# Kernel tuning notes

Measured on AMD Instinct MI355X. Metric: run time of the kernel, lower is better.

Reference implementation:

```python
import jax, jax.numpy as jnp
import numpy as np

N, E = 50000, 800000
F_IN, H = 64, 64
DEPTH, LAYERS = 3, 2


def setup_inputs() -> dict:
    key = jax.random.key(0)
    ks = jax.random.split(key, 14)
    z = jax.random.normal(ks[0], (N, F_IN), dtype=jnp.float32)
    edge_index = jax.random.randint(ks[1], (2, E), 0, N, dtype=jnp.int64)
    s = 1.0 / np.sqrt(H)
    u = lambda k, shape: jax.random.uniform(k, shape, jnp.float32, -s, s)
    return dict(
        z=z, edge_index=edge_index,
        # GRU layer 0 (input F_IN), torch gate order r,z,n
        W_ih0=u(ks[2], (3 * H, F_IN)), W_hh0=u(ks[3], (3 * H, H)),
        b_ih0=u(ks[4], (3 * H,)), b_hh0=u(ks[5], (3 * H,)),
        # GRU layer 1 (input H)
        W_ih1=u(ks[6], (3 * H, H)), W_hh1=u(ks[7], (3 * H, H)),
        b_ih1=u(ks[8], (3 * H,)), b_hh1=u(ks[9], (3 * H,)),
        # output head: Tanh -> Linear(H, 1)
        W_out=u(ks[10], (1, H)), b_out=u(ks[11], (1,)),
    )


def _mean_aggr(h, src, dst, n_nodes):
    # scatter-mean of neighbor (src) states into dst nodes
    msg = jax.ops.segment_sum(h[src], dst, num_segments=n_nodes)  # [N, F]
    cnt = jax.ops.segment_sum(jnp.ones((src.shape[0],), h.dtype), dst,
                              num_segments=n_nodes)
    return msg / jnp.maximum(cnt, 1.0)[:, None]


def _gru_cell(x, h, W_ih, W_hh, b_ih, b_hh):
    gi = x @ W_ih.T + b_ih          # [N, 3H]
    gh = h @ W_hh.T + b_hh
    i_r, i_z, i_n = jnp.split(gi, 3, axis=-1)
    h_r, h_z, h_n = jnp.split(gh, 3, axis=-1)
    r = jax.nn.sigmoid(i_r + h_r)
    zt = jax.nn.sigmoid(i_z + h_z)
    n = jnp.tanh(i_n + r * h_n)
    return (1.0 - zt) * n + zt * h


def _run_gru_layer(xs, W_ih, W_hh, b_ih, b_hh):
    # xs: [T, N, F]; returns (outputs [T, N, H], last hidden [N, H])
    h0 = jnp.zeros((xs.shape[1], W_hh.shape[1]), xs.dtype)

    def step(h, x):
        h2 = _gru_cell(x, h, W_ih, W_hh, b_ih, b_hh)
        return h2, h2

    hT, ys = jax.lax.scan(step, h0, xs)
    return ys, hT


def reference(z, edge_index, W_ih0, W_hh0, b_ih0, b_hh0,
              W_ih1, W_hh1, b_ih1, b_hh1, W_out, b_out):
    src, dst = edge_index[0], edge_index[1]
    n_nodes = z.shape[0]
    # Build the tree-depth sequence: original z followed by DEPTH rounds of
    # mean message passing (irregular gather-aggregate-scatter per depth).
    seq = [z]
    h = z
    for _ in range(DEPTH):
        h = _mean_aggr(h, src, dst, n_nodes)
        seq.append(h)
    xs = jnp.stack(seq, axis=0)  # [DEPTH+1, N, F_IN]
    ys, _ = _run_gru_layer(xs, W_ih0, W_hh0, b_ih0, b_hh0)
    _, hT = _run_gru_layer(ys, W_ih1, W_hh1, b_ih1, b_hh1)  # top layer final state
    return jnp.tanh(hT) @ W_out.T + b_out  # [N, 1]
```

## Files before the change

kernel.cpp:

```cpp
#include <hip/hip_runtime.h>
#include <hip/hip_bf16.h>

#define N_NODES 50000
#define N_EDGES 800000

typedef __attribute__((ext_vector_type(8))) short short8;
typedef __attribute__((ext_vector_type(4))) float f32x4;

__device__ __forceinline__ unsigned short f2bf_hi(float f) {
    unsigned u = __float_as_uint(f);
    unsigned r = u + 0x7fffu + ((u >> 16) & 1u);
    return (unsigned short)(r >> 16);
}
__device__ __forceinline__ float bf2f(unsigned short h) {
    return __uint_as_float(((unsigned)h) << 16);
}
__device__ __forceinline__ float u2f(unsigned u) { return __uint_as_float(u); }

__device__ __forceinline__ unsigned pack_bf2(float a, float b) {
    float2 t{a, b};
    __hip_bfloat162 r = __float22bfloat162_rn(t);
    return *reinterpret_cast<unsigned*>(&r);
}

__device__ __forceinline__ float sigm_(float v) {
    return __builtin_amdgcn_rcpf(1.0f + __expf(-v));
}
__device__ __forceinline__ float tanh2_(float a) {
    float e = __expf(-2.0f * a);
    return fmaf(2.0f, __builtin_amdgcn_rcpf(1.0f + e), -1.0f);
}


__global__ __launch_bounds__(256) void count_kernel(const int* __restrict__ ei,
                                                    int* __restrict__ deg) {
    int e = blockIdx.x * 256 + threadIdx.x;
    if (e < N_EDGES) atomicAdd(&deg[ei[N_EDGES + e]], 1);
}

__global__ __launch_bounds__(256) void scan_part(const int* __restrict__ deg,
                                                 int* __restrict__ part) {
    __shared__ int sm[256];
    int b = blockIdx.x, t = threadIdx.x;
    int s = 0;
#pragma unroll
    for (int i = 0; i < 4; ++i) {
        int idx = b * 1024 + i * 256 + t;
        if (idx < N_NODES) s += deg[idx];
    }
    sm[t] = s;
    __syncthreads();
    for (int off = 128; off; off >>= 1) {
        if (t < off) sm[t] += sm[t + off];
        __syncthreads();
    }
    if (t == 0) part[b] = sm[0];
}

__global__ __launch_bounds__(1024) void scan_final(const int* __restrict__ deg,
                                                   const int* __restrict__ part,
                                                   int* __restrict__ rowptr,
                                                   int* __restrict__ cur) {
    __shared__ int sm[1024];
    __shared__ int basep;
    int b = blockIdx.x, t = threadIdx.x;
    if (t < 64) {
        int v = (t < b) ? part[t] : 0;
#pragma unroll
        for (int off = 1; off < 64; off <<= 1) v += __shfl_xor(v, off);
        if (t == 0) basep = v;
    }
    int idx = b * 1024 + t;
    int d = (idx < N_NODES) ? deg[idx] : 0;
    sm[t] = d;
    __syncthreads();
    for (int off = 1; off < 1024; off <<= 1) {
        int u = (t >= off) ? sm[t - off] : 0;
        __syncthreads();
        sm[t] += u;
        __syncthreads();
    }
    int excl = basep + sm[t] - d;
    if (idx < N_NODES) {
        rowptr[idx] = excl;
        cur[idx] = excl;
    } else if (idx == N_NODES) {
        rowptr[idx] = excl;
    }
}

__global__ __launch_bounds__(256) void fill_kernel(const int* __restrict__ ei,
                                                   int* __restrict__ cur,
                                                   int* __restrict__ col) {
    int e = blockIdx.x * 256 + threadIdx.x;
    if (e < N_EDGES) {
        int s = ei[e];
        int d = ei[N_EDGES + e];
        int p = atomicAdd(&cur[d], 1);
        col[p] = s;
    }
}


__global__ __launch_bounds__(256) void gather_f32_kernel(
    const int* __restrict__ rowptr, const int* __restrict__ col,
    const float* __restrict__ src,
    unsigned short* __restrict__ dsthi, unsigned short* __restrict__ dstlo) {
    int node = (blockIdx.x * 256 + threadIdx.x) >> 6;
    if (node >= N_NODES) return;
    const int lane = threadIdx.x & 63;
    const int g = lane >> 4;
    const int l16 = lane & 15;
    const int beg = rowptr[node], end = rowptr[node + 1];
    const float4* s4 = reinterpret_cast<const float4*>(src);

    float4 a0 = {0.f, 0.f, 0.f, 0.f}, a1 = {0.f, 0.f, 0.f, 0.f};
    float4 a2 = {0.f, 0.f, 0.f, 0.f}, a3 = {0.f, 0.f, 0.f, 0.f};
#pragma unroll 1
    for (int e = beg + 4 * g; e < end; e += 16) {
        float4 v0 = s4[col[e] * 16 + l16];
        a0.x += v0.x; a0.y += v0.y; a0.z += v0.z; a0.w += v0.w;
        if (e + 1 < end) {
            float4 v1 = s4[col[e + 1] * 16 + l16];
            a1.x += v1.x; a1.y += v1.y; a1.z += v1.z; a1.w += v1.w;
        }
        if (e + 2 < end) {
            float4 v2 = s4[col[e + 2] * 16 + l16];
            a2.x += v2.x; a2.y += v2.y; a2.z += v2.z; a2.w += v2.w;
        }
        if (e + 3 < end) {
            float4 v3 = s4[col[e + 3] * 16 + l16];
            a3.x += v3.x; a3.y += v3.y; a3.z += v3.z; a3.w += v3.w;
        }
    }
    a0.x += a1.x; a0.y += a1.y; a0.z += a1.z; a0.w += a1.w;
    a2.x += a3.x; a2.y += a3.y; a2.z += a3.z; a2.w += a3.w;
    a0.x += a2.x; a0.y += a2.y; a0.z += a2.z; a0.w += a2.w;
#pragma unroll
    for (int m = 16; m <= 32; m <<= 1) {
        a0.x += __shfl_xor(a0.x, m);
        a0.y += __shfl_xor(a0.y, m);
        a0.z += __shfl_xor(a0.z, m);
        a0.w += __shfl_xor(a0.w, m);
    }
    if (g == 0) {
        float inv = __builtin_amdgcn_rcpf(fmaxf((float)(end - beg), 1.0f));
        float m0 = a0.x * inv, m1 = a0.y * inv, m2 = a0.z * inv, m3 = a0.w * inv;
        unsigned h01 = pack_bf2(m0, m1), h23 = pack_bf2(m2, m3);
        float l0 = m0 - u2f(h01 << 16), l1 = m1 - u2f(h01 & 0xffff0000u);
        float l2 = m2 - u2f(h23 << 16), l3 = m3 - u2f(h23 & 0xffff0000u);
        uint2 hw = {h01, h23};
        uint2 lw = {pack_bf2(l0, l1), pack_bf2(l2, l3)};
        reinterpret_cast<uint2*>(dsthi)[node * 16 + l16] = hw;
        reinterpret_cast<uint2*>(dstlo)[node * 16 + l16] = lw;
    }
}


__global__ __launch_bounds__(256) void gather_bf16_kernel(
    const int* __restrict__ rowptr, const int* __restrict__ col,
    const unsigned short* __restrict__ srchi,
    unsigned short* __restrict__ dsthi, unsigned short* __restrict__ dstlo) {
    int node = (blockIdx.x * 256 + threadIdx.x) >> 6;
    if (node >= N_NODES) return;
    const int lane = threadIdx.x & 63;
    const int g = lane >> 4;
    const int l16 = lane & 15;
    const int beg = rowptr[node], end = rowptr[node + 1];
    const uint2* s2 = reinterpret_cast<const uint2*>(srchi);

    float b0 = 0.f, b1 = 0.f, b2 = 0.f, b3 = 0.f;
    float c0 = 0.f, c1 = 0.f, c2 = 0.f, c3 = 0.f;
#pragma unroll 1
    for (int e = beg + 2 * g; e < end; e += 8) {
        uint2 v = s2[col[e] * 16 + l16];
        b0 += u2f(v.x << 16); b1 += u2f(v.x & 0xffff0000u);
        b2 += u2f(v.y << 16); b3 += u2f(v.y & 0xffff0000u);
        if (e + 1 < end) {
            uint2 w = s2[col[e + 1] * 16 + l16];
            c0 += u2f(w.x << 16); c1 += u2f(w.x & 0xffff0000u);
            c2 += u2f(w.y << 16); c3 += u2f(w.y & 0xffff0000u);
        }
    }
    b0 += c0; b1 += c1; b2 += c2; b3 += c3;
#pragma unroll
    for (int m = 16; m <= 32; m <<= 1) {
        b0 += __shfl_xor(b0, m);
        b1 += __shfl_xor(b1, m);
        b2 += __shfl_xor(b2, m);
        b3 += __shfl_xor(b3, m);
    }
    if (g == 0) {
        float inv = __builtin_amdgcn_rcpf(fmaxf((float)(end - beg), 1.0f));
        float m0 = b0 * inv, m1 = b1 * inv, m2 = b2 * inv, m3 = b3 * inv;
        unsigned h01 = pack_bf2(m0, m1), h23 = pack_bf2(m2, m3);
        float l0 = m0 - u2f(h01 << 16), l1 = m1 - u2f(h01 & 0xffff0000u);
        float l2 = m2 - u2f(h23 << 16), l3 = m3 - u2f(h23 & 0xffff0000u);
        uint2 hw = {h01, h23};
        uint2 lw = {pack_bf2(l0, l1), pack_bf2(l2, l3)};
        reinterpret_cast<uint2*>(dsthi)[node * 16 + l16] = hw;
        reinterpret_cast<uint2*>(dstlo)[node * 16 + l16] = lw;
    }
}


__global__ __launch_bounds__(256) void wprep_kernel(
    const float* __restrict__ Wih0, const float* __restrict__ Whh0,
    const float* __restrict__ Wih1, const float* __restrict__ Whh1,
    unsigned short* __restrict__ wout) {
    int idx = blockIdx.x * 256 + threadIdx.x;
    if (idx >= 49152) return;
    int e = idx & 7;
    int lane = (idx >> 3) & 63;
    int ks = (idx >> 9) & 1;
    int r = idx >> 10;
    int ct = r % 12;
    int mat = (r / 12) & 1;
    int layer = r / 24;
    const float* W = layer ? (mat ? Whh1 : Wih1) : (mat ? Whh0 : Wih0);
    int j = ct * 16 + (lane & 15);
    int k = ks * 32 + ((lane >> 4) << 3) + e;
    float v = W[j * 64 + k];
    unsigned short hi = f2bf_hi(v);
    unsigned short lo = f2bf_hi(v - bf2f(hi));
    int base = layer * 49152 + mat * 24576 + ct * 2048 + ks * 1024;
    wout[base + lane * 8 + e] = hi;
    wout[base + 512 + lane * 8 + e] = lo;
}


__device__ __forceinline__ f32x4 mfma_bf16(short8 a, short8 b, f32x4 c) {
    return __builtin_amdgcn_mfma_f32_16x16x32_bf16(a, b, c, 0, 0, 0);
}

__device__ __forceinline__ short8 lds_read8(const unsigned short* p) {
    union { uint2 u[2]; short8 s; } t;
    t.u[0] = *reinterpret_cast<const uint2*>(p);
    t.u[1] = *reinterpret_cast<const uint2*>(p + 4);
    return t.s;
}

#define HPAD 76

template <int LAYER>
__device__ __forceinline__ void mfma_phase(
    int ct, int col16, int kgrp,
    const short8 (&wf)[2][2][2][2],
    float bias_a, float bias_b,
    const unsigned short (*Ahi)[HPAD], const unsigned short (*Alo)[HPAD],
    unsigned short (&Hhi)[2][32][HPAD], unsigned short (&Hlo)[2][32][HPAD],
    float (&G)[32][196], float (&Gn2)[32][68]) {
    f32x4 acc_a[2], acc_b[2];
#pragma unroll
    for (int rt = 0; rt < 2; ++rt) {
        acc_a[rt] = {bias_a, bias_a, bias_a, bias_a};
        acc_b[rt] = {bias_b, bias_b, bias_b, bias_b};
    }
#pragma unroll
    for (int rt = 0; rt < 2; ++rt) {
#pragma unroll
        for (int ks = 0; ks < 2; ++ks) {
            const int row = rt * 16 + col16;
            const int koff = ks * 32 + kgrp;
            short8 a_in_hi = lds_read8(&Ahi[row][koff]);
            short8 a_in_lo = lds_read8(&Alo[row][koff]);
            short8 a_h_hi = lds_read8(&Hhi[LAYER][row][koff]);
            short8 a_h_lo = lds_read8(&Hlo[LAYER][row][koff]);
            short8 bi0 = wf[LAYER][0][ks][0], bi1 = wf[LAYER][0][ks][1];
            short8 bh0 = wf[LAYER][1][ks][0], bh1 = wf[LAYER][1][ks][1];
            acc_a[rt] = mfma_bf16(a_in_hi, bi0, acc_a[rt]);
            acc_a[rt] = mfma_bf16(a_in_hi, bi1, acc_a[rt]);
            acc_a[rt] = mfma_bf16(a_in_lo, bi0, acc_a[rt]);
            if (ct < 8) {
                acc_a[rt] = mfma_bf16(a_h_hi, bh0, acc_a[rt]);
                acc_a[rt] = mfma_bf16(a_h_hi, bh1, acc_a[rt]);
                acc_a[rt] = mfma_bf16(a_h_lo, bh0, acc_a[rt]);
            } else {
                acc_b[rt] = mfma_bf16(a_h_hi, bh0, acc_b[rt]);
                acc_b[rt] = mfma_bf16(a_h_hi, bh1, acc_b[rt]);
                acc_b[rt] = mfma_bf16(a_h_lo, bh0, acc_b[rt]);
            }
        }
    }
    const int q4 = (kgrp >> 3) * 4;
    const int gcol = ct * 16 + col16;
#pragma unroll
    for (int rt = 0; rt < 2; ++rt) {
#pragma unroll
        for (int v = 0; v < 4; ++v) {
            int grow = rt * 16 + q4 + v;
            G[grow][gcol] = acc_a[rt][v];
            if (ct >= 8) Gn2[grow][gcol - 128] = acc_b[rt][v];
        }
    }
}

template <int LAYER>
__device__ __forceinline__ void ew_pair(
    int p,
    unsigned short (&Hhi)[2][32][HPAD], unsigned short (&Hlo)[2][32][HPAD],
    float (&G)[32][196], float (&Gn2)[32][68]) {
    int m = p >> 5, j0 = (p & 31) * 2;
    float2 gr = *reinterpret_cast<const float2*>(&G[m][j0]);
    float2 gz = *reinterpret_cast<const float2*>(&G[m][64 + j0]);
    float2 gn = *reinterpret_cast<const float2*>(&G[m][128 + j0]);
    float2 gm = *reinterpret_cast<const float2*>(&Gn2[m][j0]);
    unsigned hhi = *reinterpret_cast<const unsigned*>(&Hhi[LAYER][m][j0]);
    unsigned hlo = *reinterpret_cast<const unsigned*>(&Hlo[LAYER][m][j0]);
    float hold0 = u2f(hhi << 16) + u2f(hlo << 16);
    float hold1 = u2f(hhi & 0xffff0000u) + u2f(hlo & 0xffff0000u);
    float r0 = sigm_(gr.x), r1 = sigm_(gr.y);
    float z0 = sigm_(gz.x), z1 = sigm_(gz.y);
    float n0 = tanh2_(fmaf(r0, gm.x, gn.x));
    float n1 = tanh2_(fmaf(r1, gm.y, gn.y));
    float h0 = fmaf(z0, hold0 - n0, n0);
    float h1 = fmaf(z1, hold1 - n1, n1);
    unsigned phi = pack_bf2(h0, h1);
    float l0 = h0 - u2f(phi << 16);
    float l1 = h1 - u2f(phi & 0xffff0000u);
    unsigned plo = pack_bf2(l0, l1);
    *reinterpret_cast<unsigned*>(&Hhi[LAYER][m][j0]) = phi;
    *reinterpret_cast<unsigned*>(&Hlo[LAYER][m][j0]) = plo;
}

__device__ __forceinline__ void stage_pair_f32(const float* __restrict__ xp, int nodebase,
                                               int p,
                                               unsigned short (&Xhi)[32][HPAD],
                                               unsigned short (&Xlo)[32][HPAD]) {
    int m = p >> 5, k0 = (p & 31) * 2;
    int node = nodebase + m;
    if (node >= N_NODES) node = N_NODES - 1;
    float2 v = *reinterpret_cast<const float2*>(xp + (size_t)node * 64 + k0);
    unsigned phi = pack_bf2(v.x, v.y);
    float l0 = v.x - u2f(phi << 16);
    float l1 = v.y - u2f(phi & 0xffff0000u);
    *reinterpret_cast<unsigned*>(&Xhi[m][k0]) = phi;
    *reinterpret_cast<unsigned*>(&Xlo[m][k0]) = pack_bf2(l0, l1);
}

__global__ __launch_bounds__(768) void gru_kernel(
    const float* __restrict__ z,
    const unsigned* __restrict__ xh1, const unsigned* __restrict__ xl1,
    const unsigned* __restrict__ xh2, const unsigned* __restrict__ xl2,
    const unsigned* __restrict__ xh3, const unsigned* __restrict__ xl3,
    const unsigned short* __restrict__ wprep,
    const float* __restrict__ bih0, const float* __restrict__ bhh0,
    const float* __restrict__ bih1, const float* __restrict__ bhh1,
    const float* __restrict__ Wout, const float* __restrict__ bout,
    float* __restrict__ out) {
    __shared__ __align__(16) float G[32][196];
    __shared__ __align__(16) float Gn2[32][68];
    __shared__ __align__(16) unsigned short Hhi[2][32][HPAD];
    __shared__ __align__(16) unsigned short Hlo[2][32][HPAD];
    __shared__ __align__(16) unsigned short Xhi[32][HPAD];
    __shared__ __align__(16) unsigned short Xlo[32][HPAD];

    const int tid = threadIdx.x;
    const int lane = tid & 63;
    const int ct = tid >> 6;
    const int col16 = lane & 15;
    const int kgrp = (lane >> 4) << 3;
    const int nodebase = blockIdx.x * 32;

    short8 wf[2][2][2][2];
    {
        const short8* wp = reinterpret_cast<const short8*>(wprep);
#pragma unroll
        for (int layer = 0; layer < 2; ++layer)
#pragma unroll
            for (int mat = 0; mat < 2; ++mat)
#pragma unroll
                for (int ks = 0; ks < 2; ++ks)
#pragma unroll
                    for (int term = 0; term < 2; ++term)
                        wf[layer][mat][ks][term] =
                            wp[(layer * 49152 + mat * 24576 + ct * 2048 +
                                ks * 1024 + term * 512 + lane * 8) >> 3];
    }
    const int gcol = ct * 16 + col16;
    float bias0_a, bias0_b, bias1_a, bias1_b;
    if (ct < 8) {
        bias0_a = bih0[gcol] + bhh0[gcol]; bias0_b = 0.0f;
        bias1_a = bih1[gcol] + bhh1[gcol]; bias1_b = 0.0f;
    } else {
        bias0_a = bih0[gcol]; bias0_b = bhh0[gcol];
        bias1_a = bih1[gcol]; bias1_b = bhh1[gcol];
    }

    {
        unsigned* h32 = reinterpret_cast<unsigned*>(&Hhi[0][0][0]);
        unsigned* l32 = reinterpret_cast<unsigned*>(&Hlo[0][0][0]);
        for (int i = tid; i < 2432; i += 768) {
            h32[i] = 0;
            l32[i] = 0;
        }
    }
    stage_pair_f32(z, nodebase, tid, Xhi, Xlo);
    if (tid < 256) stage_pair_f32(z, nodebase, tid + 768, Xhi, Xlo);
    __syncthreads();

#pragma unroll 1
    for (int t = 0; t < 4; ++t) {
        mfma_phase<0>(ct, col16, kgrp, wf, bias0_a, bias0_b,
                      Xhi, Xlo, Hhi, Hlo, G, Gn2);
        __syncthreads();
        ew_pair<0>(tid, Hhi, Hlo, G, Gn2);
        if (tid < 256) ew_pair<0>(tid + 768, Hhi, Hlo, G, Gn2);
        __syncthreads();
        mfma_phase<1>(ct, col16, kgrp, wf, bias1_a, bias1_b,
                      Hhi[0], Hlo[0], Hhi, Hlo, G, Gn2);
        __syncthreads();
        if (tid < 512) {
            ew_pair<1>(tid, Hhi, Hlo, G, Gn2);
            ew_pair<1>(tid + 512, Hhi, Hlo, G, Gn2);
        } else if (t < 3) {
            const unsigned* hp = (t == 0) ? xh1 : (t == 1) ? xh2 : xh3;
            const unsigned* lp = (t == 0) ? xl1 : (t == 1) ? xl2 : xl3;
            int q = tid - 512;
#pragma unroll
            for (int i = 0; i < 4; ++i) {
                int d = q + 256 * i;
                int m = d >> 5, c = d & 31;
                int node = nodebase + m;
                if (node >= N_NODES) node = N_NODES - 1;
                *reinterpret_cast<unsigned*>(&Xhi[m][2 * c]) = hp[node * 32 + c];
                *reinterpret_cast<unsigned*>(&Xlo[m][2 * c]) = lp[node * 32 + c];
            }
        }
        __syncthreads();
    }

    if (tid < 512) {
        int m = tid >> 4, l16 = tid & 15;
        float acc = 0.0f;
#pragma unroll
        for (int q = 0; q < 4; ++q) {
            int j = l16 * 4 + q;
            float h = bf2f(Hhi[1][m][j]) + bf2f(Hlo[1][m][j]);
            acc = fmaf(tanh2_(h), Wout[j], acc);
        }
        acc += __shfl_down(acc, 8, 16);
        acc += __shfl_down(acc, 4, 16);
        acc += __shfl_down(acc, 2, 16);
        acc += __shfl_down(acc, 1, 16);
        int node = nodebase + m;
        if (l16 == 0 && node < N_NODES) out[node] = acc + bout[0];
    }
}

extern "C" void kernel_launch(void* const* d_in, const int* in_sizes, int n_in,
                              void* d_out, int out_size, void* d_ws, size_t ws_size,
                              hipStream_t stream) {
    const float* z    = (const float*)d_in[0];
    const int*   ei   = (const int*)d_in[1];
    const float* Wih0 = (const float*)d_in[2];
    const float* Whh0 = (const float*)d_in[3];
    const float* bih0 = (const float*)d_in[4];
    const float* bhh0 = (const float*)d_in[5];
    const float* Wih1 = (const float*)d_in[6];
    const float* Whh1 = (const float*)d_in[7];
    const float* bih1 = (const float*)d_in[8];
    const float* bhh1 = (const float*)d_in[9];
    const float* Wout = (const float*)d_in[10];
    const float* bout = (const float*)d_in[11];
    float* out = (float*)d_out;
    unsigned* ws = (unsigned*)d_ws;

    unsigned* xh1 = ws;
    unsigned* xl1 = xh1 + 1600000;
    unsigned* xh2 = xl1 + 1600000;
    unsigned* xl2 = xh2 + 1600000;
    unsigned* xh3 = xl2 + 1600000;
    unsigned* xl3 = xh3 + 1600000;
    unsigned short* wprep = (unsigned short*)(xl3 + 1600000);
    int* rowptr = (int*)(wprep + 98304);
    int* deg    = rowptr + 50004;
    int* cur    = deg + 50000;
    int* col    = cur + 50000;
    int* part   = col + 800000;

    hipMemsetAsync(deg, 0, 50000 * sizeof(int), stream);

    wprep_kernel<<<192, 256, 0, stream>>>(Wih0, Whh0, Wih1, Whh1, wprep);
    count_kernel<<<(N_EDGES + 255) / 256, 256, 0, stream>>>(ei, deg);
    scan_part<<<49, 256, 0, stream>>>(deg, part);
    scan_final<<<49, 1024, 0, stream>>>(deg, part, rowptr, cur);
    fill_kernel<<<(N_EDGES + 255) / 256, 256, 0, stream>>>(ei, cur, col);

    gather_f32_kernel<<<(N_NODES * 64 + 255) / 256, 256, 0, stream>>>(
        rowptr, col, z, (unsigned short*)xh1, (unsigned short*)xl1);
    gather_bf16_kernel<<<(N_NODES * 64 + 255) / 256, 256, 0, stream>>>(
        rowptr, col, (const unsigned short*)xh1,
        (unsigned short*)xh2, (unsigned short*)xl2);
    gather_bf16_kernel<<<(N_NODES * 64 + 255) / 256, 256, 0, stream>>>(
        rowptr, col, (const unsigned short*)xh2,
        (unsigned short*)xh3, (unsigned short*)xl3);

    gru_kernel<<<(N_NODES + 31) / 32, 768, 0, stream>>>(
        z, xh1, xl1, xh2, xl2, xh3, xl3, wprep,
        bih0, bhh0, bih1, bhh1, Wout, bout, out);
}
```

Baseline: 374.0 us.

## Partition neighbor gather by source range to keep source rows cache-resident

The gather kernels switch to a persistent grid in which each wave owns up to seven destination nodes and sweeps the edge lists P times. Each pass only loads source rows whose index falls in one slice of the node range, so the working set of feature rows per pass is smaller and more likely to stay in L2/MALL. The cost is re-reading col indices P times, more branch divergence, and more register pressure from seven accumulators. The bf16 gather also changes its per-lane edge stride from 2 to 4.

```diff
diff --git a/kernel.cpp b/kernel.cpp
--- a/kernel.cpp
+++ b/kernel.cpp
@@ -3,6 +3,7 @@
 
 #define N_NODES 50000
 #define N_EDGES 800000
+#define GWAVES 8192
 
 typedef __attribute__((ext_vector_type(8))) short short8;
 typedef __attribute__((ext_vector_type(4))) float f32x4;
@@ -102,104 +103,175 @@
 }
 
 
-__global__ __launch_bounds__(256) void gather_f32_kernel(
+__global__ __launch_bounds__(256, 8) void gather_f32_mp(
     const int* __restrict__ rowptr, const int* __restrict__ col,
     const float* __restrict__ src,
     unsigned short* __restrict__ dsthi, unsigned short* __restrict__ dstlo) {
-    int node = (blockIdx.x * 256 + threadIdx.x) >> 6;
-    if (node >= N_NODES) return;
+    const int gwave = (blockIdx.x * 256 + threadIdx.x) >> 6;
     const int lane = threadIdx.x & 63;
     const int g = lane >> 4;
     const int l16 = lane & 15;
-    const int beg = rowptr[node], end = rowptr[node + 1];
     const float4* s4 = reinterpret_cast<const float4*>(src);
 
-    float4 a0 = {0.f, 0.f, 0.f, 0.f}, a1 = {0.f, 0.f, 0.f, 0.f};
-    float4 a2 = {0.f, 0.f, 0.f, 0.f}, a3 = {0.f, 0.f, 0.f, 0.f};
+    float4 acc[7];
+#pragma unroll
+    for (int k = 0; k < 7; ++k) acc[k] = {0.f, 0.f, 0.f, 0.f};
+
+    const int P = 4;
 #pragma unroll 1
-    for (int e = beg + 4 * g; e < end; e += 16) {
-        float4 v0 = s4[col[e] * 16 + l16];
-        a0.x += v0.x; a0.y += v0.y; a0.z += v0.z; a0.w += v0.w;
-        if (e + 1 < end) {
-            float4 v1 = s4[col[e + 1] * 16 + l16];
-            a1.x += v1.x; a1.y += v1.y; a1.z += v1.z; a1.w += v1.w;
-        }
-        if (e + 2 < end) {
-            float4 v2 = s4[col[e + 2] * 16 + l16];
-            a2.x += v2.x; a2.y += v2.y; a2.z += v2.z; a2.w += v2.w;
-        }
-        if (e + 3 < end) {
-            float4 v3 = s4[col[e + 3] * 16 + l16];
-            a3.x += v3.x; a3.y += v3.y; a3.z += v3.z; a3.w += v3.w;
-        }
-    }
-    a0.x += a1.x; a0.y += a1.y; a0.z += a1.z; a0.w += a1.w;
-    a2.x += a3.x; a2.y += a3.y; a2.z += a3.z; a2.w += a3.w;
-    a0.x += a2.x; a0.y += a2.y; a0.z += a2.z; a0.w += a2.w;
-#pragma unroll
-    for (int m = 16; m <= 32; m <<= 1) {
-        a0.x += __shfl_xor(a0.x, m);
-        a0.y += __shfl_xor(a0.y, m);
-        a0.z += __shfl_xor(a0.z, m);
-        a0.w += __shfl_xor(a0.w, m);
-    }
-    if (g == 0) {
-        float inv = __builtin_amdgcn_rcpf(fmaxf((float)(end - beg), 1.0f));
-        float m0 = a0.x * inv, m1 = a0.y * inv, m2 = a0.z * inv, m3 = a0.w * inv;
-        unsigned h01 = pack_bf2(m0, m1), h23 = pack_bf2(m2, m3);
-        float l0 = m0 - u2f(h01 << 16), l1 = m1 - u2f(h01 & 0xffff0000u);
-        float l2 = m2 - u2f(h23 << 16), l3 = m3 - u2f(h23 & 0xffff0000u);
-        uint2 hw = {h01, h23};
-        uint2 lw = {pack_bf2(l0, l1), pack_bf2(l2, l3)};
-        reinterpret_cast<uint2*>(dsthi)[node * 16 + l16] = hw;
-        reinterpret_cast<uint2*>(dstlo)[node * 16 + l16] = lw;
-    }
-}
-
-
-__global__ __launch_bounds__(256) void gather_bf16_kernel(
+    for (int p = 0; p < P; ++p) {
+        const int lo = (int)(((long long)N_NODES * p) / P);
+        const int hi = (int)(((long long)N_NODES * (p + 1)) / P);
+#pragma unroll
+        for (int k = 0; k < 7; ++k) {
+            int node = gwave + k * GWAVES;
+            if (node >= N_NODES) break;
+            const int beg = rowptr[node], end = rowptr[node + 1];
+#pragma unroll 1
+            for (int e = beg + 4 * g; e < end; e += 16) {
+                int c0 = col[e];
+                if (c0 >= lo && c0 < hi) {
+                    float4 v = s4[c0 * 16 + l16];
+                    acc[k].x += v.x; acc[k].y += v.y;
+                    acc[k].z += v.z; acc[k].w += v.w;
+                }
+                if (e + 1 < end) {
+                    int c1 = col[e + 1];
+                    if (c1 >= lo && c1 < hi) {
+                        float4 v = s4[c1 * 16 + l16];
+                        acc[k].x += v.x; acc[k].y += v.y;
+                        acc[k].z += v.z; acc[k].w += v.w;
+                    }
+                }
+                if (e + 2 < end) {
+                    int c2 = col[e + 2];
+                    if (c2 >= lo && c2 < hi) {
+                        float4 v = s4[c2 * 16 + l16];
+                        acc[k].x += v.x; acc[k].y += v.y;
+                        acc[k].z += v.z; acc[k].w += v.w;
+                    }
+                }
+                if (e + 3 < end) {
+                    int c3 = col[e + 3];
+                    if (c3 >= lo && c3 < hi) {
+                        float4 v = s4[c3 * 16 + l16];
+                        acc[k].x += v.x; acc[k].y += v.y;
+                        acc[k].z += v.z; acc[k].w += v.w;
+                    }
+                }
+            }
+        }
+    }
+#pragma unroll
+    for (int k = 0; k < 7; ++k) {
+        int node = gwave + k * GWAVES;
+        if (node >= N_NODES) break;
+        float4 a = acc[k];
+#pragma unroll
+        for (int m = 16; m <= 32; m <<= 1) {
+            a.x += __shfl_xor(a.x, m);
+            a.y += __shfl_xor(a.y, m);
+            a.z += __shfl_xor(a.z, m);
+            a.w += __shfl_xor(a.w, m);
+        }
+        if (g == 0) {
+            const int beg = rowptr[node], end = rowptr[node + 1];
+            float inv = __builtin_amdgcn_rcpf(fmaxf((float)(end - beg), 1.0f));
+            float m0 = a.x * inv, m1 = a.y * inv, m2 = a.z * inv, m3 = a.w * inv;
+            unsigned h01 = pack_bf2(m0, m1), h23 = pack_bf2(m2, m3);
+            float l0 = m0 - u2f(h01 << 16), l1 = m1 - u2f(h01 & 0xffff0000u);
+            float l2 = m2 - u2f(h23 << 16), l3 = m3 - u2f(h23 & 0xffff0000u);
+            uint2 hw = {h01, h23};
+            uint2 lw = {pack_bf2(l0, l1), pack_bf2(l2, l3)};
+            reinterpret_cast<uint2*>(dsthi)[node * 16 + l16] = hw;
+            reinterpret_cast<uint2*>(dstlo)[node * 16 + l16] = lw;
+        }
+    }
+}
+
+__global__ __launch_bounds__(256, 8) void gather_bf16_mp(
     const int* __restrict__ rowptr, const int* __restrict__ col,
     const unsigned short* __restrict__ srchi,
     unsigned short* __restrict__ dsthi, unsigned short* __restrict__ dstlo) {
-    int node = (blockIdx.x * 256 + threadIdx.x) >> 6;
-    if (node >= N_NODES) return;
+    const int gwave = (blockIdx.x * 256 + threadIdx.x) >> 6;
     const int lane = threadIdx.x & 63;
     const int g = lane >> 4;
     const int l16 = lane & 15;
-    const int beg = rowptr[node], end = rowptr[node + 1];
     const uint2* s2 = reinterpret_cast<const uint2*>(srchi);
 
-    float b0 = 0.f, b1 = 0.f, b2 = 0.f, b3 = 0.f;
-    float c0 = 0.f, c1 = 0.f, c2 = 0.f, c3 = 0.f;
+    float4 acc[7];
+#pragma unroll
+    for (int k = 0; k < 7; ++k) acc[k] = {0.f, 0.f, 0.f, 0.f};
+
+    const int P = 3;
 #pragma unroll 1
-    for (int e = beg + 2 * g; e < end; e += 8) {
-        uint2 v = s2[col[e] * 16 + l16];
-        b0 += u2f(v.x << 16); b1 += u2f(v.x & 0xffff0000u);
-        b2 += u2f(v.y << 16); b3 += u2f(v.y & 0xffff0000u);
-        if (e + 1 < end) {
-            uint2 w = s2[col[e + 1] * 16 + l16];
-            c0 += u2f(w.x << 16); c1 += u2f(w.x & 0xffff0000u);
-            c2 += u2f(w.y << 16); c3 += u2f(w.y & 0xffff0000u);
-        }
-    }
-    b0 += c0; b1 += c1; b2 += c2; b3 += c3;
-#pragma unroll
-    for (int m = 16; m <= 32; m <<= 1) {
-        b0 += __shfl_xor(b0, m);
-        b1 += __shfl_xor(b1, m);
-        b2 += __shfl_xor(b2, m);
-        b3 += __shfl_xor(b3, m);
-    }
-    if (g == 0) {
-        float inv = __builtin_amdgcn_rcpf(fmaxf((float)(end - beg), 1.0f));
-        float m0 = b0 * inv, m1 = b1 * inv, m2 = b2 * inv, m3 = b3 * inv;
-        unsigned h01 = pack_bf2(m0, m1), h23 = pack_bf2(m2, m3);
-        float l0 = m0 - u2f(h01 << 16), l1 = m1 - u2f(h01 & 0xffff0000u);
-        float l2 = m2 - u2f(h23 << 16), l3 = m3 - u2f(h23 & 0xffff0000u);
-        uint2 hw = {h01, h23};
-        uint2 lw = {pack_bf2(l0, l1), pack_bf2(l2, l3)};
-        reinterpret_cast<uint2*>(dsthi)[node * 16 + l16] = hw;
-        reinterpret_cast<uint2*>(dstlo)[node * 16 + l16] = lw;
+    for (int p = 0; p < P; ++p) {
+        const int lo = (int)(((long long)N_NODES * p) / P);
+        const int hi = (int)(((long long)N_NODES * (p + 1)) / P);
+#pragma unroll
+        for (int k = 0; k < 7; ++k) {
+            int node = gwave + k * GWAVES;
+            if (node >= N_NODES) break;
+            const int beg = rowptr[node], end = rowptr[node + 1];
+#pragma unroll 1
+            for (int e = beg + 4 * g; e < end; e += 16) {
+                int c0 = col[e];
+                if (c0 >= lo && c0 < hi) {
+                    uint2 v = s2[c0 * 16 + l16];
+                    acc[k].x += u2f(v.x << 16); acc[k].y += u2f(v.x & 0xffff0000u);
+                    acc[k].z += u2f(v.y << 16); acc[k].w += u2f(v.y & 0xffff0000u);
+                }
+                if (e + 1 < end) {
+                    int c1 = col[e + 1];
+                    if (c1 >= lo && c1 < hi) {
+                        uint2 v = s2[c1 * 16 + l16];
+                        acc[k].x += u2f(v.x << 16); acc[k].y += u2f(v.x & 0xffff0000u);
+                        acc[k].z += u2f(v.y << 16); acc[k].w += u2f(v.y & 0xffff0000u);
+                    }
+                }
+                if (e + 2 < end) {
+                    int c2 = col[e + 2];
+                    if (c2 >= lo && c2 < hi) {
+                        uint2 v = s2[c2 * 16 + l16];
+                        acc[k].x += u2f(v.x << 16); acc[k].y += u2f(v.x & 0xffff0000u);
+                        acc[k].z += u2f(v.y << 16); acc[k].w += u2f(v.y & 0xffff0000u);
+                    }
+                }
+                if (e + 3 < end) {
+                    int c3 = col[e + 3];
+                    if (c3 >= lo && c3 < hi) {
+                        uint2 v = s2[c3 * 16 + l16];
+                        acc[k].x += u2f(v.x << 16); acc[k].y += u2f(v.x & 0xffff0000u);
+                        acc[k].z += u2f(v.y << 16); acc[k].w += u2f(v.y & 0xffff0000u);
+                    }
+                }
+            }
+        }
+    }
+#pragma unroll
+    for (int k = 0; k < 7; ++k) {
+        int node = gwave + k * GWAVES;
+        if (node >= N_NODES) break;
+        float4 a = acc[k];
+#pragma unroll
+        for (int m = 16; m <= 32; m <<= 1) {
+            a.x += __shfl_xor(a.x, m);
+            a.y += __shfl_xor(a.y, m);
+            a.z += __shfl_xor(a.z, m);
+            a.w += __shfl_xor(a.w, m);
+        }
+        if (g == 0) {
+            const int beg = rowptr[node], end = rowptr[node + 1];
+            float inv = __builtin_amdgcn_rcpf(fmaxf((float)(end - beg), 1.0f));
+            float m0 = a.x * inv, m1 = a.y * inv, m2 = a.z * inv, m3 = a.w * inv;
+            unsigned h01 = pack_bf2(m0, m1), h23 = pack_bf2(m2, m3);
+            float l0 = m0 - u2f(h01 << 16), l1 = m1 - u2f(h01 & 0xffff0000u);
+            float l2 = m2 - u2f(h23 << 16), l3 = m3 - u2f(h23 & 0xffff0000u);
+            uint2 hw = {h01, h23};
+            uint2 lw = {pack_bf2(l0, l1), pack_bf2(l2, l3)};
+            reinterpret_cast<uint2*>(dsthi)[node * 16 + l16] = hw;
+            reinterpret_cast<uint2*>(dstlo)[node * 16 + l16] = lw;
+        }
     }
 }
 
@@ -487,14 +559,12 @@
     scan_final<<<49, 1024, 0, stream>>>(deg, part, rowptr, cur);
     fill_kernel<<<(N_EDGES + 255) / 256, 256, 0, stream>>>(ei, cur, col);
 
-    gather_f32_kernel<<<(N_NODES * 64 + 255) / 256, 256, 0, stream>>>(
-        rowptr, col, z, (unsigned short*)xh1, (unsigned short*)xl1);
-    gather_bf16_kernel<<<(N_NODES * 64 + 255) / 256, 256, 0, stream>>>(
-        rowptr, col, (const unsigned short*)xh1,
-        (unsigned short*)xh2, (unsigned short*)xl2);
-    gather_bf16_kernel<<<(N_NODES * 64 + 255) / 256, 256, 0, stream>>>(
-        rowptr, col, (const unsigned short*)xh2,
-        (unsigned short*)xh3, (unsigned short*)xl3);
+    gather_f32_mp<<<2048, 256, 0, stream>>>(rowptr, col, z,
+        (unsigned short*)xh1, (unsigned short*)xl1);
+    gather_bf16_mp<<<2048, 256, 0, stream>>>(rowptr, col,
+        (const unsigned short*)xh1, (unsigned short*)xh2, (unsigned short*)xl2);
+    gather_bf16_mp<<<2048, 256, 0, stream>>>(rowptr, col,
+        (const unsigned short*)xh2, (unsigned short*)xh3, (unsigned short*)xl3);
 
     gru_kernel<<<(N_NODES + 31) / 32, 768, 0, stream>>>(
         z, xh1, xl1, xh2, xl2, xh3, xl3, wprep,
```

New measurement: 507.6 us. 35.7% more time.

## Split gather feature arrays into column slabs to shrink per-pass working set

Applied to the files above, without the earlier changes.

Node features are reorganised into column slabs (16 floats or 16 packed bf16 pairs per node per slab), and each gather pass processes one slab at a time across separate block ranges. This is meant to make the randomly accessed source slab small enough to stay resident in cache while neighbors are gathered, cutting DRAM traffic from irregular reads. It adds a transpose kernel for z, more blocks and narrower per-lane loads, repeated reads of rowptr/col per slab, and a slab-addressed load in the GRU kernel.

```diff
diff --git a/kernel.cpp b/kernel.cpp
--- a/kernel.cpp
+++ b/kernel.cpp
@@ -3,6 +3,7 @@
 
 #define N_NODES 50000
 #define N_EDGES 800000
+#define SLABU 800000
 
 typedef __attribute__((ext_vector_type(8))) short short8;
 typedef __attribute__((ext_vector_type(4))) float f32x4;
@@ -102,104 +103,97 @@
 }
 
 
-__global__ __launch_bounds__(256) void gather_f32_kernel(
+__global__ __launch_bounds__(256) void zslab_kernel(const float* __restrict__ z,
+                                                    float* __restrict__ zs) {
+    int idx = blockIdx.x * 256 + threadIdx.x;
+    if (idx < N_NODES * 64) {
+        int node = idx >> 6, f = idx & 63;
+        zs[(f >> 4) * SLABU + node * 16 + (f & 15)] = z[idx];
+    }
+}
+
+
+__global__ __launch_bounds__(256) void gather_f32_slab(
     const int* __restrict__ rowptr, const int* __restrict__ col,
-    const float* __restrict__ src,
-    unsigned short* __restrict__ dsthi, unsigned short* __restrict__ dstlo) {
-    int node = (blockIdx.x * 256 + threadIdx.x) >> 6;
-    if (node >= N_NODES) return;
+    const float* __restrict__ zs,
+    unsigned* __restrict__ dsthi, unsigned* __restrict__ dstlo) {
+    const int b = blockIdx.x;
+    const int s = b / 12500;
+    const int node = (b % 12500) * 4 + (threadIdx.x >> 6);
     const int lane = threadIdx.x & 63;
     const int g = lane >> 4;
     const int l16 = lane & 15;
+    const float* src = zs + (size_t)s * SLABU + l16;
     const int beg = rowptr[node], end = rowptr[node + 1];
-    const float4* s4 = reinterpret_cast<const float4*>(src);
-
-    float4 a0 = {0.f, 0.f, 0.f, 0.f}, a1 = {0.f, 0.f, 0.f, 0.f};
-    float4 a2 = {0.f, 0.f, 0.f, 0.f}, a3 = {0.f, 0.f, 0.f, 0.f};
+
+    float a0 = 0.f, a1 = 0.f, a2 = 0.f, a3 = 0.f;
 #pragma unroll 1
     for (int e = beg + 4 * g; e < end; e += 16) {
-        float4 v0 = s4[col[e] * 16 + l16];
-        a0.x += v0.x; a0.y += v0.y; a0.z += v0.z; a0.w += v0.w;
-        if (e + 1 < end) {
-            float4 v1 = s4[col[e + 1] * 16 + l16];
-            a1.x += v1.x; a1.y += v1.y; a1.z += v1.z; a1.w += v1.w;
-        }
-        if (e + 2 < end) {
-            float4 v2 = s4[col[e + 2] * 16 + l16];
-            a2.x += v2.x; a2.y += v2.y; a2.z += v2.z; a2.w += v2.w;
-        }
-        if (e + 3 < end) {
-            float4 v3 = s4[col[e + 3] * 16 + l16];
-            a3.x += v3.x; a3.y += v3.y; a3.z += v3.z; a3.w += v3.w;
-        }
-    }
-    a0.x += a1.x; a0.y += a1.y; a0.z += a1.z; a0.w += a1.w;
-    a2.x += a3.x; a2.y += a3.y; a2.z += a3.z; a2.w += a3.w;
-    a0.x += a2.x; a0.y += a2.y; a0.z += a2.z; a0.w += a2.w;
-#pragma unroll
-    for (int m = 16; m <= 32; m <<= 1) {
-        a0.x += __shfl_xor(a0.x, m);
-        a0.y += __shfl_xor(a0.y, m);
-        a0.z += __shfl_xor(a0.z, m);
-        a0.w += __shfl_xor(a0.w, m);
-    }
-    if (g == 0) {
-        float inv = __builtin_amdgcn_rcpf(fmaxf((float)(end - beg), 1.0f));
-        float m0 = a0.x * inv, m1 = a0.y * inv, m2 = a0.z * inv, m3 = a0.w * inv;
-        unsigned h01 = pack_bf2(m0, m1), h23 = pack_bf2(m2, m3);
-        float l0 = m0 - u2f(h01 << 16), l1 = m1 - u2f(h01 & 0xffff0000u);
-        float l2 = m2 - u2f(h23 << 16), l3 = m3 - u2f(h23 & 0xffff0000u);
-        uint2 hw = {h01, h23};
-        uint2 lw = {pack_bf2(l0, l1), pack_bf2(l2, l3)};
-        reinterpret_cast<uint2*>(dsthi)[node * 16 + l16] = hw;
-        reinterpret_cast<uint2*>(dstlo)[node * 16 + l16] = lw;
-    }
-}
-
-
-__global__ __launch_bounds__(256) void gather_bf16_kernel(
+        a0 += src[col[e] * 16];
+        if (e + 1 < end) a1 += src[col[e + 1] * 16];
+        if (e + 2 < end) a2 += src[col[e + 2] * 16];
+        if (e + 3 < end) a3 += src[col[e + 3] * 16];
+    }
+    a0 = (a0 + a1) + (a2 + a3);
+    a0 += __shfl_xor(a0, 16);
+    a0 += __shfl_xor(a0, 32);
+    float inv = __builtin_amdgcn_rcpf(fmaxf((float)(end - beg), 1.0f));
+    float f = a0 * inv;
+    float fn = __shfl_down(f, 1);
+    if (g == 0 && !(l16 & 1)) {
+        unsigned ph = pack_bf2(f, fn);
+        float le = f - u2f(ph << 16);
+        float lo_ = fn - u2f(ph & 0xffff0000u);
+        unsigned pl = pack_bf2(le, lo_);
+        int o = (s >> 1) * SLABU + node * 16 + (s & 1) * 8 + (l16 >> 1);
+        dsthi[o] = ph;
+        dstlo[o] = pl;
+    }
+}
+
+
+__global__ __launch_bounds__(256) void gather_bf16_slab(
     const int* __restrict__ rowptr, const int* __restrict__ col,
-    const unsigned short* __restrict__ srchi,
-    unsigned short* __restrict__ dsthi, unsigned short* __restrict__ dstlo) {
-    int node = (blockIdx.x * 256 + threadIdx.x) >> 6;
-    if (node >= N_NODES) return;
+    const unsigned* __restrict__ srchi,
+    unsigned* __restrict__ dsthi, unsigned* __restrict__ dstlo) {
+    const int b = blockIdx.x;
+    const int s = b / 12500;
+    const int node = (b % 12500) * 4 + (threadIdx.x >> 6);
     const int lane = threadIdx.x & 63;
     const int g = lane >> 4;
     const int l16 = lane & 15;
+    const unsigned* src = srchi + (size_t)s * SLABU + l16;
     const int beg = rowptr[node], end = rowptr[node + 1];
-    const uint2* s2 = reinterpret_cast<const uint2*>(srchi);
-
-    float b0 = 0.f, b1 = 0.f, b2 = 0.f, b3 = 0.f;
-    float c0 = 0.f, c1 = 0.f, c2 = 0.f, c3 = 0.f;
+
+    float a0 = 0.f, a1 = 0.f, b0 = 0.f, b1 = 0.f;
 #pragma unroll 1
     for (int e = beg + 2 * g; e < end; e += 8) {
-        uint2 v = s2[col[e] * 16 + l16];
-        b0 += u2f(v.x << 16); b1 += u2f(v.x & 0xffff0000u);
-        b2 += u2f(v.y << 16); b3 += u2f(v.y & 0xffff0000u);
+        unsigned v = src[col[e] * 16];
+        a0 += u2f(v << 16);
+        a1 += u2f(v & 0xffff0000u);
         if (e + 1 < end) {
-            uint2 w = s2[col[e + 1] * 16 + l16];
-            c0 += u2f(w.x << 16); c1 += u2f(w.x & 0xffff0000u);
-            c2 += u2f(w.y << 16); c3 += u2f(w.y & 0xffff0000u);
-        }
-    }
-    b0 += c0; b1 += c1; b2 += c2; b3 += c3;
+            unsigned w = src[col[e + 1] * 16];
+            b0 += u2f(w << 16);
+            b1 += u2f(w & 0xffff0000u);
+        }
+    }
+    a0 += b0;
+    a1 += b1;
 #pragma unroll
     for (int m = 16; m <= 32; m <<= 1) {
-        b0 += __shfl_xor(b0, m);
-        b1 += __shfl_xor(b1, m);
-        b2 += __shfl_xor(b2, m);
-        b3 += __shfl_xor(b3, m);
+        a0 += __shfl_xor(a0, m);
+        a1 += __shfl_xor(a1, m);
     }
     if (g == 0) {
         float inv = __builtin_amdgcn_rcpf(fmaxf((float)(end - beg), 1.0f));
-        float m0 = b0 * inv, m1 = b1 * inv, m2 = b2 * inv, m3 = b3 * inv;
-        unsigned h01 = pack_bf2(m0, m1), h23 = pack_bf2(m2, m3);
-        float l0 = m0 - u2f(h01 << 16), l1 = m1 - u2f(h01 & 0xffff0000u);
-        float l2 = m2 - u2f(h23 << 16), l3 = m3 - u2f(h23 & 0xffff0000u);
-        uint2 hw = {h01, h23};
-        uint2 lw = {pack_bf2(l0, l1), pack_bf2(l2, l3)};
-        reinterpret_cast<uint2*>(dsthi)[node * 16 + l16] = hw;
-        reinterpret_cast<uint2*>(dstlo)[node * 16 + l16] = lw;
+        float m0 = a0 * inv, m1 = a1 * inv;
+        unsigned ph = pack_bf2(m0, m1);
+        float l0 = m0 - u2f(ph << 16);
+        float l1 = m1 - u2f(ph & 0xffff0000u);
+        unsigned pl = pack_bf2(l0, l1);
+        int o = s * SLABU + node * 16 + l16;
+        dsthi[o] = ph;
+        dstlo[o] = pl;
     }
 }
 
@@ -423,8 +417,9 @@
                 int m = d >> 5, c = d & 31;
                 int node = nodebase + m;
                 if (node >= N_NODES) node = N_NODES - 1;
-                *reinterpret_cast<unsigned*>(&Xhi[m][2 * c]) = hp[node * 32 + c];
-                *reinterpret_cast<unsigned*>(&Xlo[m][2 * c]) = lp[node * 32 + c];
+                int addr = (c >> 4) * SLABU + node * 16 + (c & 15);
+                *reinterpret_cast<unsigned*>(&Xhi[m][2 * c]) = hp[addr];
+                *reinterpret_cast<unsigned*>(&Xlo[m][2 * c]) = lp[addr];
             }
         }
         __syncthreads();
@@ -472,7 +467,8 @@
     unsigned* xl2 = xh2 + 1600000;
     unsigned* xh3 = xl2 + 1600000;
     unsigned* xl3 = xh3 + 1600000;
-    unsigned short* wprep = (unsigned short*)(xl3 + 1600000);
+    float* zs = (float*)(xl3 + 1600000);
+    unsigned short* wprep = (unsigned short*)(zs + 3200000);
     int* rowptr = (int*)(wprep + 98304);
     int* deg    = rowptr + 50004;
     int* cur    = deg + 50000;
@@ -482,19 +478,15 @@
     hipMemsetAsync(deg, 0, 50000 * sizeof(int), stream);
 
     wprep_kernel<<<192, 256, 0, stream>>>(Wih0, Whh0, Wih1, Whh1, wprep);
+    zslab_kernel<<<12500, 256, 0, stream>>>(z, zs);
     count_kernel<<<(N_EDGES + 255) / 256, 256, 0, stream>>>(ei, deg);
     scan_part<<<49, 256, 0, stream>>>(deg, part);
     scan_final<<<49, 1024, 0, stream>>>(deg, part, rowptr, cur);
     fill_kernel<<<(N_EDGES + 255) / 256, 256, 0, stream>>>(ei, cur, col);
 
-    gather_f32_kernel<<<(N_NODES * 64 + 255) / 256, 256, 0, stream>>>(
-        rowptr, col, z, (unsigned short*)xh1, (unsigned short*)xl1);
-    gather_bf16_kernel<<<(N_NODES * 64 + 255) / 256, 256, 0, stream>>>(
-        rowptr, col, (const unsigned short*)xh1,
-        (unsigned short*)xh2, (unsigned short*)xl2);
-    gather_bf16_kernel<<<(N_NODES * 64 + 255) / 256, 256, 0, stream>>>(
-        rowptr, col, (const unsigned short*)xh2,
-        (unsigned short*)xh3, (unsigned short*)xl3);
+    gather_f32_slab<<<50000, 256, 0, stream>>>(rowptr, col, zs, xh1, xl1);
+    gather_bf16_slab<<<25000, 256, 0, stream>>>(rowptr, col, xh1, xh2, xl2);
+    gather_bf16_slab<<<25000, 256, 0, stream>>>(rowptr, col, xh2, xh3, xl3);
 
     gru_kernel<<<(N_NODES + 31) / 32, 768, 0, stream>>>(
         z, xh1, xl1, xh2, xl2, xh3, xl3, wprep,
```

Measured after the change: 468.9 us. 1.25x slower.

## Fuse GRU elementwise update into n-gate MFMA waves via register accumulators

Applied to the files above, without the earlier changes.

The n-gate waves (ct>=8) now keep their input and hidden n-gate accumulators in registers and compute the GRU elementwise update themselves, reading only the r/z gates from a smaller shared G buffer. This drops the Gn2 buffer and the shared-memory round trip for the n gates. The other 8 waves take over staging of the next timestep's inputs. The elementwise work is now spread over 4 of 12 waves instead of all of them, which trades fewer LDS writes for less parallelism in that phase.

```diff
diff --git a/kernel.cpp b/kernel.cpp
--- a/kernel.cpp
+++ b/kernel.cpp
@@ -249,7 +249,7 @@
     float bias_a, float bias_b,
     const unsigned short (*Ahi)[HPAD], const unsigned short (*Alo)[HPAD],
     unsigned short (&Hhi)[2][32][HPAD], unsigned short (&Hlo)[2][32][HPAD],
-    float (&G)[32][196], float (&Gn2)[32][68]) {
+    float (&G)[32][132], f32x4 (&na)[2], f32x4 (&nb)[2]) {
     f32x4 acc_a[2], acc_b[2];
 #pragma unroll
     for (int rt = 0; rt < 2; ++rt) {
@@ -282,45 +282,47 @@
             }
         }
     }
+    if (ct < 8) {
+        const int q4 = (kgrp >> 3) * 4;
+        const int gcol = ct * 16 + col16;
+#pragma unroll
+        for (int rt = 0; rt < 2; ++rt)
+#pragma unroll
+            for (int v = 0; v < 4; ++v)
+                G[rt * 16 + q4 + v][gcol] = acc_a[rt][v];
+    } else {
+#pragma unroll
+        for (int rt = 0; rt < 2; ++rt) {
+            na[rt] = acc_a[rt];
+            nb[rt] = acc_b[rt];
+        }
+    }
+}
+
+template <int LAYER>
+__device__ __forceinline__ void ew_nwave(
+    int ct, int col16, int kgrp,
+    const f32x4 (&na)[2], const f32x4 (&nb)[2],
+    unsigned short (&Hhi)[2][32][HPAD], unsigned short (&Hlo)[2][32][HPAD],
+    float (&G)[32][132]) {
+    if (ct < 8) return;
+    const int f = (ct - 8) * 16 + col16;
     const int q4 = (kgrp >> 3) * 4;
-    const int gcol = ct * 16 + col16;
 #pragma unroll
     for (int rt = 0; rt < 2; ++rt) {
 #pragma unroll
         for (int v = 0; v < 4; ++v) {
-            int grow = rt * 16 + q4 + v;
-            G[grow][gcol] = acc_a[rt][v];
-            if (ct >= 8) Gn2[grow][gcol - 128] = acc_b[rt][v];
-        }
-    }
-}
-
-template <int LAYER>
-__device__ __forceinline__ void ew_pair(
-    int p,
-    unsigned short (&Hhi)[2][32][HPAD], unsigned short (&Hlo)[2][32][HPAD],
-    float (&G)[32][196], float (&Gn2)[32][68]) {
-    int m = p >> 5, j0 = (p & 31) * 2;
-    float2 gr = *reinterpret_cast<const float2*>(&G[m][j0]);
-    float2 gz = *reinterpret_cast<const float2*>(&G[m][64 + j0]);
-    float2 gn = *reinterpret_cast<const float2*>(&G[m][128 + j0]);
-    float2 gm = *reinterpret_cast<const float2*>(&Gn2[m][j0]);
-    unsigned hhi = *reinterpret_cast<const unsigned*>(&Hhi[LAYER][m][j0]);
-    unsigned hlo = *reinterpret_cast<const unsigned*>(&Hlo[LAYER][m][j0]);
-    float hold0 = u2f(hhi << 16) + u2f(hlo << 16);
-    float hold1 = u2f(hhi & 0xffff0000u) + u2f(hlo & 0xffff0000u);
-    float r0 = sigm_(gr.x), r1 = sigm_(gr.y);
-    float z0 = sigm_(gz.x), z1 = sigm_(gz.y);
-    float n0 = tanh2_(fmaf(r0, gm.x, gn.x));
-    float n1 = tanh2_(fmaf(r1, gm.y, gn.y));
-    float h0 = fmaf(z0, hold0 - n0, n0);
-    float h1 = fmaf(z1, hold1 - n1, n1);
-    unsigned phi = pack_bf2(h0, h1);
-    float l0 = h0 - u2f(phi << 16);
-    float l1 = h1 - u2f(phi & 0xffff0000u);
-    unsigned plo = pack_bf2(l0, l1);
-    *reinterpret_cast<unsigned*>(&Hhi[LAYER][m][j0]) = phi;
-    *reinterpret_cast<unsigned*>(&Hlo[LAYER][m][j0]) = plo;
+            int m = rt * 16 + q4 + v;
+            float rr = sigm_(G[m][f]);
+            float zz = sigm_(G[m][64 + f]);
+            float nn = tanh2_(fmaf(rr, nb[rt][v], na[rt][v]));
+            float hold = bf2f(Hhi[LAYER][m][f]) + bf2f(Hlo[LAYER][m][f]);
+            float h = fmaf(zz, hold - nn, nn);
+            unsigned short hi = f2bf_hi(h);
+            Hhi[LAYER][m][f] = hi;
+            Hlo[LAYER][m][f] = f2bf_hi(h - bf2f(hi));
+        }
+    }
 }
 
 __device__ __forceinline__ void stage_pair_f32(const float* __restrict__ xp, int nodebase,
@@ -348,8 +350,7 @@
     const float* __restrict__ bih1, const float* __restrict__ bhh1,
     const float* __restrict__ Wout, const float* __restrict__ bout,
     float* __restrict__ out) {
-    __shared__ __align__(16) float G[32][196];
-    __shared__ __align__(16) float Gn2[32][68];
+    __shared__ __align__(16) float G[32][132];
     __shared__ __align__(16) unsigned short Hhi[2][32][HPAD];
     __shared__ __align__(16) unsigned short Hlo[2][32][HPAD];
     __shared__ __align__(16) unsigned short Xhi[32][HPAD];
@@ -399,27 +400,25 @@
     if (tid < 256) stage_pair_f32(z, nodebase, tid + 768, Xhi, Xlo);
     __syncthreads();
 
+    f32x4 na[2], nb[2];
+
 #pragma unroll 1
     for (int t = 0; t < 4; ++t) {
         mfma_phase<0>(ct, col16, kgrp, wf, bias0_a, bias0_b,
-                      Xhi, Xlo, Hhi, Hlo, G, Gn2);
-        __syncthreads();
-        ew_pair<0>(tid, Hhi, Hlo, G, Gn2);
-        if (tid < 256) ew_pair<0>(tid + 768, Hhi, Hlo, G, Gn2);
+                      Xhi, Xlo, Hhi, Hlo, G, na, nb);
+        __syncthreads();
+        ew_nwave<0>(ct, col16, kgrp, na, nb, Hhi, Hlo, G);
         __syncthreads();
         mfma_phase<1>(ct, col16, kgrp, wf, bias1_a, bias1_b,
-                      Hhi[0], Hlo[0], Hhi, Hlo, G, Gn2);
-        __syncthreads();
-        if (tid < 512) {
-            ew_pair<1>(tid, Hhi, Hlo, G, Gn2);
-            ew_pair<1>(tid + 512, Hhi, Hlo, G, Gn2);
-        } else if (t < 3) {
+                      Hhi[0], Hlo[0], Hhi, Hlo, G, na, nb);
+        __syncthreads();
+        ew_nwave<1>(ct, col16, kgrp, na, nb, Hhi, Hlo, G);
+        if (ct < 8 && t < 3) {
             const unsigned* hp = (t == 0) ? xh1 : (t == 1) ? xh2 : xh3;
             const unsigned* lp = (t == 0) ? xl1 : (t == 1) ? xl2 : xl3;
-            int q = tid - 512;
-#pragma unroll
-            for (int i = 0; i < 4; ++i) {
-                int d = q + 256 * i;
+#pragma unroll
+            for (int i = 0; i < 2; ++i) {
+                int d = tid + 512 * i;
                 int m = d >> 5, c = d & 31;
                 int node = nodebase + m;
                 if (node >= N_NODES) node = N_NODES - 1;
```

Result: slower. 396.9 us (+6.1%).
